# Kernel tuning notes

Measured on AMD Instinct MI355X. Metric: run time of the kernel, lower is better.

## Reference

```python
import jax, jax.numpy as jnp
import numpy as np

B, M, L, S = 16, 128, 32, 512
D, H, DFF, NL = 768, 12, 3072, 4
NE = 50000
HD = D // H
EPS = 1e-5


def _ln(x, w, b):
    mu = jnp.mean(x, axis=-1, keepdims=True)
    var = jnp.var(x, axis=-1, keepdims=True)
    return (x - mu) * jax.lax.rsqrt(var + EPS) * w + b


def setup_inputs() -> dict:
    key = jax.random.key(0)
    ks = jax.random.split(key, 24)
    sd = 0.02
    lens = jax.random.randint(ks[1], (B, M), 1, L + 1)
    pos = jax.random.randint(ks[2], (B, M, L), 0, S)
    pos = jnp.where(jnp.arange(L)[None, None, :] < lens[..., None], pos, -1)
    return {
        "last_hidden_state": jax.random.normal(ks[0], (B, S, D), jnp.float32),
        "entity_position_ids": pos.astype(jnp.int64),
        "entity_attention_mask": jax.random.randint(ks[3], (B, M), 0, 2).astype(jnp.int64),
        "attn_w": jax.random.normal(ks[4], (D,), jnp.float32) * sd,
        "attn_b": jnp.zeros((), jnp.float32),
        "qkv_w": jax.random.normal(ks[5], (NL, 3 * D, D), jnp.float32) * sd,
        "qkv_b": jnp.zeros((NL, 3 * D), jnp.float32),
        "out_w": jax.random.normal(ks[6], (NL, D, D), jnp.float32) * sd,
        "out_b": jnp.zeros((NL, D), jnp.float32),
        "ln1_w": jnp.ones((NL, D), jnp.float32),
        "ln1_b": jnp.zeros((NL, D), jnp.float32),
        "ff1_w": jax.random.normal(ks[7], (NL, DFF, D), jnp.float32) * sd,
        "ff1_b": jnp.zeros((NL, DFF), jnp.float32),
        "ff2_w": jax.random.normal(ks[8], (NL, D, DFF), jnp.float32) * sd,
        "ff2_b": jnp.zeros((NL, D), jnp.float32),
        "ln2_w": jnp.ones((NL, D), jnp.float32),
        "ln2_b": jnp.zeros((NL, D), jnp.float32),
        "cls_w1": jax.random.normal(ks[9], (100, D), jnp.float32) * sd,
        "cls_w2": jax.random.normal(ks[10], (NE, 100), jnp.float32) * sd,
        "cls_b2": jnp.zeros((NE,), jnp.float32),
    }


def reference(last_hidden_state, entity_position_ids, entity_attention_mask,
              attn_w, attn_b, qkv_w, qkv_b, out_w, out_b, ln1_w, ln1_b,
              ff1_w, ff1_b, ff2_w, ff2_b, ln2_w, ln2_b, cls_w1, cls_w2, cls_b2):
    # Ragged mention fill (vectorized form of the triple python loop).
    # Original code writes last_hidden_state[i, x, :] (loop index x, not the
    # position id) until the first -1 in entity_position_ids[i, j, :].
    not_break = jnp.cumprod((entity_position_ids != -1).astype(jnp.int32), axis=-1)  # [B,M,L]
    valid = (entity_attention_mask != 0)[:, :, None].astype(jnp.int32) * not_break   # [B,M,L]
    mentions = valid[..., None].astype(last_hidden_state.dtype) * \
        last_hidden_state[:, None, :L, :]  # [B,M,L,D]

    # attention pooling over mention length
    logits = jnp.einsum('bmld,d->bml', mentions, attn_w) + attn_b
    scores = jax.nn.softmax(logits, axis=-1)
    x = jnp.einsum('bml,bmld->bmd', scores, mentions)  # [B,M,D]

    scale = 1.0 / np.sqrt(HD)
    for i in range(NL):
        qkv = x @ qkv_w[i].T + qkv_b[i]  # [B,M,3D]
        q, k, v = jnp.split(qkv, 3, axis=-1)
        q = q.reshape(B, M, H, HD).transpose(0, 2, 1, 3)
        k = k.reshape(B, M, H, HD).transpose(0, 2, 1, 3)
        v = v.reshape(B, M, H, HD).transpose(0, 2, 1, 3)
        attn = jax.nn.softmax(jnp.einsum('bhqd,bhkd->bhqk', q, k) * scale, axis=-1)
        ao = jnp.einsum('bhqk,bhkd->bhqd', attn, v).transpose(0, 2, 1, 3).reshape(B, M, D)
        ao = ao @ out_w[i].T + out_b[i]
        x = _ln(x + ao, ln1_w[i], ln1_b[i])
        ff = jax.nn.relu(x @ ff1_w[i].T + ff1_b[i]) @ ff2_w[i].T + ff2_b[i]
        x = _ln(x + ff, ln2_w[i], ln2_b[i])

    return (x @ cls_w1.T) @ cls_w2.T + cls_b2  # [B,M,NE]
```

## Files before the change

### kernel.cpp

```cpp
#include <hip/hip_runtime.h>
#include <math.h>

#define NBATCH 16
#define NMENT  128
#define NM     2048
#define LSEQ   32
#define SSEQ   512
#define DD     768
#define NHEAD  12
#define HDIM   64
#define DFF    3072
#define NLAYER 4
#define NENT   50000

typedef __bf16 bf16;
typedef __attribute__((__ext_vector_type__(4))) float f32x4;
typedef __attribute__((__ext_vector_type__(8))) bf16 bf16x8;
typedef __attribute__((__ext_vector_type__(4))) bf16 bf16x4;

__device__ __forceinline__ void gl2lds16(const bf16* g, bf16* l) {
  __builtin_amdgcn_global_load_lds(
      (const __attribute__((address_space(1))) void*)g,
      (__attribute__((address_space(3))) void*)l, 16, 0, 0);
}

#define C_QKV (NLAYER * 3 * DD * DD / 4)
#define C_OUT (NLAYER * DD * DD / 4)
#define C_FF  (NLAYER * DFF * DD / 4)
#define C_W1  (128 * DD)
#define C_W2  (50048 * 128)
#define C_TOTAL (C_QKV + C_OUT + 2 * C_FF + C_W1 + C_W2)

__device__ __forceinline__ void cvt4(const float* s, bf16* d, int i) {
  const float4 v = ((const float4*)s)[i];
  bf16x4 o;
  o.x = (bf16)v.x; o.y = (bf16)v.y; o.z = (bf16)v.z; o.w = (bf16)v.w;
  ((bf16x4*)d)[i] = o;
}

__global__ __launch_bounds__(256) void conv_all(
    const float* __restrict__ qkv_w, const float* __restrict__ out_w,
    const float* __restrict__ ff1_w, const float* __restrict__ ff2_w,
    const float* __restrict__ cls_w1, const float* __restrict__ cls_w2,
    bf16* __restrict__ Wqkv, bf16* __restrict__ Wout, bf16* __restrict__ Wff1,
    bf16* __restrict__ Wff2, bf16* __restrict__ Wc1, bf16* __restrict__ Wc2) {
  int i = blockIdx.x * 256 + threadIdx.x;
  if (i < C_QKV) { cvt4(qkv_w, Wqkv, i); return; }
  i -= C_QKV;
  if (i < C_OUT) { cvt4(out_w, Wout, i); return; }
  i -= C_OUT;
  if (i < C_FF) { cvt4(ff1_w, Wff1, i); return; }
  i -= C_FF;
  if (i < C_FF) { cvt4(ff2_w, Wff2, i); return; }
  i -= C_FF;
  if (i < C_W1) {
    const int r = i / DD;
    Wc1[i] = (bf16)((r < 100) ? cls_w1[i] : 0.f);
    return;
  }
  i -= C_W1;
  if (i < C_W2) {
    const int r = i >> 7, c = i & 127;
    const float v = (r < NENT && c < 100) ? cls_w2[r * 100 + c] : 0.f;
    Wc2[i] = (bf16)v;
  }
}

__global__ __launch_bounds__(256) void red4_bf16(const float* __restrict__ p,
                                                 bf16* __restrict__ d, int n4) {
  const int i = blockIdx.x * 256 + threadIdx.x;
  if (i >= n4) return;
  const float4 a = ((const float4*)p)[i];
  const float4 b = ((const float4*)p)[i + (size_t)n4];
  const float4 c = ((const float4*)p)[i + 2 * (size_t)n4];
  const float4 e = ((const float4*)p)[i + 3 * (size_t)n4];
  bf16x4 o;
  o.x = (bf16)(a.x + b.x + c.x + e.x);
  o.y = (bf16)(a.y + b.y + c.y + e.y);
  o.z = (bf16)(a.z + b.z + c.z + e.z);
  o.w = (bf16)(a.w + b.w + c.w + e.w);
  ((bf16x4*)d)[i] = o;
}

__global__ __launch_bounds__(64) void tdot_kernel(const float* __restrict__ lhs,
                                                  const float* __restrict__ aw,
                                                  float* __restrict__ t) {
  const int bl = blockIdx.x;
  const int b = bl >> 5, l = bl & 31;
  const int lane = threadIdx.x;
  const float* row = lhs + ((size_t)b * SSEQ + l) * DD;
  float s = 0.f;
#pragma unroll
  for (int u = 0; u < DD / 64; ++u)
    s += row[lane + 64 * u] * aw[lane + 64 * u];
#pragma unroll
  for (int off = 32; off > 0; off >>= 1) s += __shfl_down(s, off);
  if (lane == 0) t[bl] = s;
}

__global__ __launch_bounds__(256) void pool_kernel(const float* __restrict__ lhs,
                                                   const int* __restrict__ pos,
                                                   const int* __restrict__ msk,
                                                   const float* __restrict__ t,
                                                   float* __restrict__ X,
                                                   bf16* __restrict__ Xb) {
  __shared__ float wgt[LSEQ];
  __shared__ int ok[LSEQ];
  const int bm = blockIdx.x;
  const int b = bm >> 7;
  const int tid = threadIdx.x;
  if (tid < LSEQ) ok[tid] = (pos[(size_t)bm * LSEQ + tid] != -1) ? 1 : 0;
  __syncthreads();
  if (tid == 0) {
    const int mk = (msk[bm] != 0) ? 1 : 0;
    int run = 1;
    float lg[LSEQ];
    int vld[LSEQ];
#pragma unroll
    for (int l = 0; l < LSEQ; ++l) {
      run &= ok[l];
      vld[l] = mk & run;
      lg[l] = vld[l] ? t[b * LSEQ + l] : 0.f;
    }
    float mx = lg[0];
#pragma unroll
    for (int l = 1; l < LSEQ; ++l) mx = fmaxf(mx, lg[l]);
    float s = 0.f;
#pragma unroll
    for (int l = 0; l < LSEQ; ++l) { lg[l] = expf(lg[l] - mx); s += lg[l]; }
    const float inv = 1.f / s;
#pragma unroll
    for (int l = 0; l < LSEQ; ++l) wgt[l] = vld[l] ? lg[l] * inv : 0.f;
  }
  __syncthreads();
#pragma unroll
  for (int u = 0; u < 3; ++u) {
    const int d = tid + 256 * u;
    float acc = 0.f;
#pragma unroll
    for (int l = 0; l < LSEQ; ++l)
      acc += wgt[l] * lhs[((size_t)b * SSEQ + l) * DD + d];
    X[(size_t)bm * DD + d] = acc;
    Xb[(size_t)bm * DD + d] = (bf16)acc;
  }
}

template <int OUT_BF16, int RELU, int HAS_BIAS, int GUARD_N>
__global__ __launch_bounds__(256) void gemm_mfma(const bf16* __restrict__ A,
                                                 const bf16* __restrict__ B,
                                                 const float* __restrict__ bias,
                                                 void* __restrict__ Cp,
                                                 int K, int lda, int ldb,
                                                 int ldc, int ncols) {
  __shared__ __align__(16) bf16 As[2][128 * 32];
  __shared__ __align__(16) bf16 Bs[2][128 * 32];
  const int tid = threadIdx.x;
  const int wave = tid >> 6, lane = tid & 63;
  const int rb = blockIdx.y * 128, cb = blockIdx.x * 128;
  const int wm = (wave >> 1) * 64, wn = (wave & 1) * 64;
  const int koff = blockIdx.z * K;

  const int sr = wave * 32 + (lane >> 2);
  const int sk = (lane & 3) * 8;
  const bf16* ga0 = A + (size_t)(rb + sr) * lda + koff + sk;
  const bf16* ga1 = A + (size_t)(rb + sr + 16) * lda + koff + sk;
  const bf16* gb0 = B + (size_t)(cb + sr) * ldb + koff + sk;
  const bf16* gb1 = B + (size_t)(cb + sr + 16) * ldb + koff + sk;
  const int so = wave * 1024;

  const int fr = lane & 15, fk = (lane >> 4) * 8;

  f32x4 acc[4][4];
#pragma unroll
  for (int i = 0; i < 4; ++i)
#pragma unroll
    for (int j = 0; j < 4; ++j) acc[i][j] = (f32x4)0.f;

  gl2lds16(ga0, &As[0][so]); gl2lds16(ga1, &As[0][so + 512]);
  gl2lds16(gb0, &Bs[0][so]); gl2lds16(gb1, &Bs[0][so + 512]);
  ga0 += 32; ga1 += 32; gb0 += 32; gb1 += 32;
  __syncthreads();

  const int nsteps = K >> 5;
  int cur = 0;
  for (int t = 0; t < nsteps; ++t) {
    if (t + 1 < nsteps) {
      const int nxt = cur ^ 1;
      gl2lds16(ga0, &As[nxt][so]); gl2lds16(ga1, &As[nxt][so + 512]);
      gl2lds16(gb0, &Bs[nxt][so]); gl2lds16(gb1, &Bs[nxt][so + 512]);
      ga0 += 32; ga1 += 32; gb0 += 32; gb1 += 32;
    }
    __builtin_amdgcn_sched_barrier(0);
    bf16x8 af[4], bfr[4];
#pragma unroll
    for (int i = 0; i < 4; ++i)
      af[i] = *(const bf16x8*)(&As[cur][(wm + i * 16 + fr) * 32 + fk]);
#pragma unroll
    for (int j = 0; j < 4; ++j)
      bfr[j] = *(const bf16x8*)(&Bs[cur][(wn + j * 16 + fr) * 32 + fk]);
#pragma unroll
    for (int i = 0; i < 4; ++i)
#pragma unroll
      for (int j = 0; j < 4; ++j)
        acc[i][j] = __builtin_amdgcn_mfma_f32_16x16x32_bf16(af[i], bfr[j],
                                                            acc[i][j], 0, 0, 0);
    __syncthreads();
    cur ^= 1;
  }

  const size_t zoff = (size_t)blockIdx.z * (size_t)(gridDim.y << 7) * ldc;
  const int r0 = rb + wm + ((lane >> 4) << 2);
  const int c0 = cb + wn + fr;
#pragma unroll
  for (int i = 0; i < 4; ++i) {
#pragma unroll
    for (int j = 0; j < 4; ++j) {
      const int col = c0 + j * 16;
      if (GUARD_N && col >= ncols) continue;
      const float bv = HAS_BIAS ? bias[col] : 0.f;
#pragma unroll
      for (int r = 0; r < 4; ++r) {
        float v = acc[i][j][r] + bv;
        if (RELU) v = fmaxf(v, 0.f);
        const int row = r0 + i * 16 + r;
        if (OUT_BF16)
          ((bf16*)Cp)[zoff + (size_t)row * ldc + col] = (bf16)v;
        else
          ((float*)Cp)[zoff + (size_t)row * ldc + col] = v;
      }
    }
  }
}

__global__ __launch_bounds__(256) void attn_kernel(const float* __restrict__ qkv,
                                                   bf16* __restrict__ ao) {
  __shared__ float smem[2 * 64 * 132 + 128 * 132];
  float* Qs = smem;
  float* Ks = smem + 64 * 132;
  float* Ps = smem + 2 * 64 * 132;
  float* Vs = smem;

  const int tid = threadIdx.x;
  const int b = blockIdx.x / NHEAD;
  const int h = blockIdx.x % NHEAD;
  const float* base = qkv + (size_t)b * NMENT * (3 * DD) + h * HDIM;

#pragma unroll
  for (int it = 0; it < 8; ++it) {
    const int idx = tid + it * 256;
    const int m = idx >> 4;
    const int d0 = (idx & 15) * 4;
    const float4 q = *(const float4*)(base + (size_t)m * (3 * DD) + d0);
    const float4 k = *(const float4*)(base + (size_t)m * (3 * DD) + DD + d0);
    Qs[(d0 + 0) * 132 + m] = q.x; Qs[(d0 + 1) * 132 + m] = q.y;
    Qs[(d0 + 2) * 132 + m] = q.z; Qs[(d0 + 3) * 132 + m] = q.w;
    Ks[(d0 + 0) * 132 + m] = k.x; Ks[(d0 + 1) * 132 + m] = k.y;
    Ks[(d0 + 2) * 132 + m] = k.z; Ks[(d0 + 3) * 132 + m] = k.w;
  }
  __syncthreads();

  const int tm = (tid >> 4) * 8;
  const int tn = (tid & 15) * 8;
  {
    float acc[8][8];
#pragma unroll
    for (int i = 0; i < 8; ++i)
#pragma unroll
      for (int j = 0; j < 8; ++j) acc[i][j] = 0.f;
    for (int d = 0; d < HDIM; ++d) {
      float a[8], bv[8];
      *(float4*)&a[0] = *(const float4*)&Qs[d * 132 + tm];
      *(float4*)&a[4] = *(const float4*)&Qs[d * 132 + tm + 4];
      *(float4*)&bv[0] = *(const float4*)&Ks[d * 132 + tn];
      *(float4*)&bv[4] = *(const float4*)&Ks[d * 132 + tn + 4];
#pragma unroll
      for (int i = 0; i < 8; ++i)
#pragma unroll
        for (int j = 0; j < 8; ++j)
          acc[i][j] = fmaf(a[i], bv[j], acc[i][j]);
    }
    const float scale = 0.125f;
#pragma unroll
    for (int i = 0; i < 8; ++i)
#pragma unroll
      for (int j = 0; j < 8; ++j)
        Ps[(tn + j) * 132 + (tm + i)] = acc[i][j] * scale;
  }
  __syncthreads();

#pragma unroll
  for (int it = 0; it < 8; ++it) {
    const int idx = tid + it * 256;
    const int m = idx >> 4;
    const int d0 = (idx & 15) * 4;
    const float4 v = *(const float4*)(base + (size_t)m * (3 * DD) + 2 * DD + d0);
    *(float4*)&Vs[m * 68 + d0] = v;
  }
  if (tid < NMENT) {
    const int r = tid;
    float mx = -1e30f;
    for (int c = 0; c < NMENT; ++c) mx = fmaxf(mx, Ps[c * 132 + r]);
    float s = 0.f;
    for (int c = 0; c < NMENT; ++c) {
      const float e = expf(Ps[c * 132 + r] - mx);
      Ps[c * 132 + r] = e;
      s += e;
    }
    const float inv = 1.f / s;
    for (int c = 0; c < NMENT; ++c) Ps[c * 132 + r] *= inv;
  }
  __syncthreads();

  const int om = (tid >> 4) * 8;
  const int od = (tid & 15) * 4;
  float oacc[8][4];
#pragma unroll
  for (int i = 0; i < 8; ++i)
#pragma unroll
    for (int j = 0; j < 4; ++j) oacc[i][j] = 0.f;
  for (int c = 0; c < NMENT; ++c) {
    float p[8];
    *(float4*)&p[0] = *(const float4*)&Ps[c * 132 + om];
    *(float4*)&p[4] = *(const float4*)&Ps[c * 132 + om + 4];
    const float4 vv = *(const float4*)&Vs[c * 68 + od];
#pragma unroll
    for (int i = 0; i < 8; ++i) {
      oacc[i][0] = fmaf(p[i], vv.x, oacc[i][0]);
      oacc[i][1] = fmaf(p[i], vv.y, oacc[i][1]);
      oacc[i][2] = fmaf(p[i], vv.z, oacc[i][2]);
      oacc[i][3] = fmaf(p[i], vv.w, oacc[i][3]);
    }
  }
#pragma unroll
  for (int i = 0; i < 8; ++i) {
    bf16x4 ov;
    ov.x = (bf16)oacc[i][0]; ov.y = (bf16)oacc[i][1];
    ov.z = (bf16)oacc[i][2]; ov.w = (bf16)oacc[i][3];
    *(bf16x4*)(ao + (size_t)(b * NMENT + om + i) * DD + h * HDIM + od) = ov;
  }
}

template <int NS>
__global__ __launch_bounds__(256) void ln_kernel(const float* __restrict__ x,
                                                 const float* __restrict__ y,
                                                 const float* __restrict__ bias,
                                                 const float* __restrict__ w,
                                                 const float* __restrict__ bb,
                                                 float* __restrict__ o,
                                                 bf16* __restrict__ ob) {
  __shared__ float red1[4], red2[4];
  __shared__ float mshare, vshare;
  const int row = blockIdx.x;
  const int tid = threadIdx.x;
  const int wave = tid >> 6, lane = tid & 63;
  const float* xr = x + (size_t)row * DD;
  const float* yr = y + (size_t)row * DD;
  float v[3];
  float s = 0.f;
#pragma unroll
  for (int u = 0; u < 3; ++u) {
    const int d = tid + 256 * u;
    float acc = xr[d] + bias[d];
#pragma unroll
    for (int n = 0; n < NS; ++n) acc += yr[(size_t)n * NM * DD + d];
    v[u] = acc;
    s += acc;
  }
#pragma unroll
  for (int off = 32; off > 0; off >>= 1) s += __shfl_down(s, off);
  if (lane == 0) red1[wave] = s;
  __syncthreads();
  if (tid == 0) mshare = (red1[0] + red1[1] + red1[2] + red1[3]) * (1.f / DD);
  __syncthreads();
  const float mean = mshare;
  float q = 0.f;
#pragma unroll
  for (int u = 0; u < 3; ++u) { const float d = v[u] - mean; q += d * d; }
#pragma unroll
  for (int off = 32; off > 0; off >>= 1) q += __shfl_down(q, off);
  if (lane == 0) red2[wave] = q;
  __syncthreads();
  if (tid == 0)
    vshare = rsqrtf((red2[0] + red2[1] + red2[2] + red2[3]) * (1.f / DD) + 1e-5f);
  __syncthreads();
  const float rstd = vshare;
  float* orow = o + (size_t)row * DD;
  bf16* brow = ob + (size_t)row * DD;
#pragma unroll
  for (int u = 0; u < 3; ++u) {
    const int d = tid + 256 * u;
    const float r = (v[u] - mean) * rstd * w[d] + bb[d];
    orow[d] = r;
    brow[d] = (bf16)r;
  }
}

extern "C" void kernel_launch(void* const* d_in, const int* in_sizes, int n_in,
                              void* d_out, int out_size, void* d_ws, size_t ws_size,
                              hipStream_t stream) {
  const float* lhs    = (const float*)d_in[0];
  const int*   pos    = (const int*)d_in[1];
  const int*   msk    = (const int*)d_in[2];
  const float* attn_w = (const float*)d_in[3];
  const float* qkv_w  = (const float*)d_in[5];
  const float* qkv_b  = (const float*)d_in[6];
  const float* out_w  = (const float*)d_in[7];
  const float* out_b  = (const float*)d_in[8];
  const float* ff1_w  = (const float*)d_in[11];
  const float* ff1_b  = (const float*)d_in[12];
  const float* ff2_w  = (const float*)d_in[13];
  const float* ff2_b  = (const float*)d_in[14];
  const float* ln1_w  = (const float*)d_in[9];
  const float* ln1_b  = (const float*)d_in[10];
  const float* ln2_w  = (const float*)d_in[15];
  const float* ln2_b  = (const float*)d_in[16];
  const float* cls_w1 = (const float*)d_in[17];
  const float* cls_w2 = (const float*)d_in[18];
  const float* cls_b2 = (const float*)d_in[19];
  float* out = (float*)d_out;

  char* p = (char*)d_ws;
  auto carve = [&](size_t bytes) {
    void* r = (void*)p;
    p += (bytes + 255) & ~(size_t)255;
    return r;
  };
  float* T    = (float*)carve(512 * 4);
  float* X    = (float*)carve((size_t)NM * DD * 4);
  float* SCR  = (float*)carve((size_t)4 * NM * DD * 4);
  bf16* Xb    = (bf16*)carve((size_t)NM * DD * 2);
  bf16* AOb   = (bf16*)carve((size_t)NM * DD * 2);
  bf16* H1    = (bf16*)carve((size_t)NM * DFF * 2);
  bf16* Hb    = (bf16*)carve((size_t)NM * 128 * 2);
  bf16* Wqkv  = (bf16*)carve((size_t)NLAYER * 3 * DD * DD * 2);
  bf16* Wout  = (bf16*)carve((size_t)NLAYER * DD * DD * 2);
  bf16* Wff1  = (bf16*)carve((size_t)NLAYER * DFF * DD * 2);
  bf16* Wff2  = (bf16*)carve((size_t)NLAYER * DD * DFF * 2);
  bf16* Wc1   = (bf16*)carve((size_t)128 * DD * 2);
  bf16* Wc2   = (bf16*)carve((size_t)50048 * 128 * 2);

  conv_all<<<(C_TOTAL + 255) / 256, 256, 0, stream>>>(
      qkv_w, out_w, ff1_w, ff2_w, cls_w1, cls_w2,
      Wqkv, Wout, Wff1, Wff2, Wc1, Wc2);

  tdot_kernel<<<NBATCH * LSEQ, 64, 0, stream>>>(lhs, attn_w, T);
  pool_kernel<<<NM, 256, 0, stream>>>(lhs, pos, msk, T, X, Xb);

  for (int i = 0; i < NLAYER; ++i) {
    gemm_mfma<0, 0, 1, 0><<<dim3(18, 16), 256, 0, stream>>>(
        Xb, Wqkv + (size_t)i * 3 * DD * DD, qkv_b + (size_t)i * 3 * DD, SCR,
        DD, DD, DD, 3 * DD, 3 * DD);
    attn_kernel<<<NBATCH * NHEAD, 256, 0, stream>>>(SCR, AOb);
    gemm_mfma<0, 0, 0, 0><<<dim3(6, 16, 2), 256, 0, stream>>>(
        AOb, Wout + (size_t)i * DD * DD, nullptr, SCR,
        DD / 2, DD, DD, DD, DD);
    ln_kernel<2><<<NM, 256, 0, stream>>>(X, SCR, out_b + (size_t)i * DD,
                                         ln1_w + (size_t)i * DD,
                                         ln1_b + (size_t)i * DD, X, Xb);
    gemm_mfma<1, 1, 1, 0><<<dim3(24, 16), 256, 0, stream>>>(
        Xb, Wff1 + (size_t)i * DFF * DD, ff1_b + (size_t)i * DFF, H1,
        DD, DD, DD, DFF, DFF);
    gemm_mfma<0, 0, 0, 0><<<dim3(6, 16, 4), 256, 0, stream>>>(
        H1, Wff2 + (size_t)i * DD * DFF, nullptr, SCR,
        DFF / 4, DFF, DFF, DD, DD);
    ln_kernel<4><<<NM, 256, 0, stream>>>(X, SCR, ff2_b + (size_t)i * DD,
                                         ln2_w + (size_t)i * DD,
                                         ln2_b + (size_t)i * DD, X, Xb);
  }

  gemm_mfma<0, 0, 0, 0><<<dim3(1, 16, 4), 256, 0, stream>>>(
      Xb, Wc1, nullptr, SCR, DD / 4, DD, DD, 128, 128);
  {
    const int n4 = NM * 128 / 4;
    red4_bf16<<<(n4 + 255) / 256, 256, 0, stream>>>(SCR, Hb, n4);
  }
  gemm_mfma<0, 0, 1, 1><<<dim3(391, 16), 256, 0, stream>>>(
      Hb, Wc2, cls_b2, out, 128, 128, 128, NENT, NENT);
}
```

Baseline: 1.121 ms.

## Triple-buffer GEMM LDS staging with explicit vmcnt waits

Moves the bf16 MFMA GEMM from double-buffered to triple-buffered LDS tiles. Two tiles are prefetched ahead, and each step waits with an explicit s_waitcnt vmcnt count instead of a full __syncthreads drain. The aim is to keep more global-to-LDS loads in flight so load latency is better hidden behind MFMA work. This costs 50% more shared memory, which may lower occupancy. The hand-written vmcnt counts and the raw s_barrier calls are fragile with respect to memory ordering.

```diff
diff --git a/kernel.cpp b/kernel.cpp
--- a/kernel.cpp
+++ b/kernel.cpp
@@ -152,8 +152,8 @@
                                                  void* __restrict__ Cp,
                                                  int K, int lda, int ldb,
                                                  int ldc, int ncols) {
-  __shared__ __align__(16) bf16 As[2][128 * 32];
-  __shared__ __align__(16) bf16 Bs[2][128 * 32];
+  __shared__ __align__(16) bf16 As[3][128 * 32];
+  __shared__ __align__(16) bf16 Bs[3][128 * 32];
   const int tid = threadIdx.x;
   const int wave = tid >> 6, lane = tid & 63;
   const int rb = blockIdx.y * 128, cb = blockIdx.x * 128;
@@ -170,27 +170,36 @@
 
   const int fr = lane & 15, fk = (lane >> 4) * 8;
 
+  const int nsteps = K >> 5;
+
+  auto stage = [&](int bsel) {
+    bf16* sa = &As[bsel][so];
+    bf16* sb = &Bs[bsel][so];
+    gl2lds16(ga0, sa); gl2lds16(ga1, sa + 512);
+    gl2lds16(gb0, sb); gl2lds16(gb1, sb + 512);
+    ga0 += 32; ga1 += 32; gb0 += 32; gb1 += 32;
+  };
+
   f32x4 acc[4][4];
 #pragma unroll
   for (int i = 0; i < 4; ++i)
 #pragma unroll
     for (int j = 0; j < 4; ++j) acc[i][j] = (f32x4)0.f;
 
-  gl2lds16(ga0, &As[0][so]); gl2lds16(ga1, &As[0][so + 512]);
-  gl2lds16(gb0, &Bs[0][so]); gl2lds16(gb1, &Bs[0][so + 512]);
-  ga0 += 32; ga1 += 32; gb0 += 32; gb1 += 32;
-  __syncthreads();
-
-  const int nsteps = K >> 5;
+  stage(0);
+  if (nsteps > 1) stage(1);
+  if (nsteps > 2) stage(2);
+
   int cur = 0;
   for (int t = 0; t < nsteps; ++t) {
-    if (t + 1 < nsteps) {
-      const int nxt = cur ^ 1;
-      gl2lds16(ga0, &As[nxt][so]); gl2lds16(ga1, &As[nxt][so + 512]);
-      gl2lds16(gb0, &Bs[nxt][so]); gl2lds16(gb1, &Bs[nxt][so + 512]);
-      ga0 += 32; ga1 += 32; gb0 += 32; gb1 += 32;
-    }
-    __builtin_amdgcn_sched_barrier(0);
+    if (t < nsteps - 2)
+      asm volatile("s_waitcnt vmcnt(8)" ::: "memory");
+    else if (t == nsteps - 2)
+      asm volatile("s_waitcnt vmcnt(4)" ::: "memory");
+    else
+      asm volatile("s_waitcnt vmcnt(0)" ::: "memory");
+    __builtin_amdgcn_s_barrier();
+
     bf16x8 af[4], bfr[4];
 #pragma unroll
     for (int i = 0; i < 4; ++i)
@@ -204,8 +213,10 @@
       for (int j = 0; j < 4; ++j)
         acc[i][j] = __builtin_amdgcn_mfma_f32_16x16x32_bf16(af[i], bfr[j],
                                                             acc[i][j], 0, 0, 0);
-    __syncthreads();
-    cur ^= 1;
+
+    __builtin_amdgcn_s_barrier();
+    if (t + 3 < nsteps) stage(cur);
+    cur = (cur == 2) ? 0 : cur + 1;
   }
 
   const size_t zoff = (size_t)blockIdx.z * (size_t)(gridDim.y << 7) * ldc;
```

Result: faster. 1.095 ms (-2.3%).
